# Optimization experiments

Hardware: AMD Instinct MI355X
Metric: run time of the kernel (lower is better)

## Reference

```python
import jax, jax.numpy as jnp
import numpy as np

T = 1024
HID = 2880
H = 64        # query heads
KVH = 8       # kv heads
G = H // KVH  # GQA group size
D = 64        # head dim
WIN = 128     # sliding window
BASE = 150000.0
INIT_CTX = 4096
SCALING = 32.0
NTK_ALPHA = 1.0
NTK_BETA = 32.0
EPS = 1e-5


def _rope_cache():
    # YaRN-style NTK rope cache (scaling_factor > 1 branch), computed in float32.
    d_half = D // 2
    freq = BASE ** (np.arange(0, D, 2, dtype=np.float64) / D)
    concentration = 0.1 * np.log(SCALING) + 1.0
    low = d_half * np.log(INIT_CTX / (NTK_BETA * 2 * np.pi)) / np.log(BASE)
    high = d_half * np.log(INIT_CTX / (NTK_ALPHA * 2 * np.pi)) / np.log(BASE)
    interpolation = 1.0 / (SCALING * freq)
    extrapolation = 1.0 / freq
    ramp = (np.arange(d_half, dtype=np.float64) - low) / (high - low)
    mask = 1.0 - np.clip(ramp, 0.0, 1.0)
    inv_freq = interpolation * (1.0 - mask) + extrapolation * mask
    t = np.arange(INIT_CTX, dtype=np.float64)
    freqs = np.outer(t, inv_freq)                  # [INIT_CTX, D/2]
    cos = (np.cos(freqs) * concentration).astype(np.float32)
    sin = (np.sin(freqs) * concentration).astype(np.float32)
    return jnp.asarray(cos), jnp.asarray(sin)

_COS, _SIN = _rope_cache()


def _apply_rope(x, cos, sin):
    # x: [T, nh, D], cos/sin: [T, D/2]
    c = cos[:, None, :]
    s = sin[:, None, :]
    x1, x2 = jnp.split(x, 2, axis=-1)
    return jnp.concatenate([x1 * c - x2 * s, x2 * c + x1 * s], axis=-1)


def setup_inputs() -> dict:
    key = jax.random.key(0)
    ks = jax.random.split(key, 8)
    hidden_states = jax.random.normal(ks[0], (T, HID), dtype=jnp.float32)
    positions = jnp.arange(T, dtype=jnp.int32)
    norm_scale = jnp.ones((HID,), dtype=jnp.float32)
    qkv_out = H * D + 2 * KVH * D  # 4096 + 512 + 512
    w_qkv = jax.random.normal(ks[1], (HID, qkv_out), dtype=jnp.float32) * (HID ** -0.5)
    b_qkv = jax.random.normal(ks[2], (qkv_out,), dtype=jnp.float32) * 0.01
    w_out = jax.random.normal(ks[3], (H * D, HID), dtype=jnp.float32) * ((H * D) ** -0.5)
    b_out = jax.random.normal(ks[4], (HID,), dtype=jnp.float32) * 0.01
    sinks = jax.random.normal(ks[5], (H,), dtype=jnp.float32)
    return {"hidden_states": hidden_states, "positions": positions,
            "norm_scale": norm_scale, "w_qkv": w_qkv, "b_qkv": b_qkv,
            "w_out": w_out, "b_out": b_out, "sinks": sinks}


def reference(hidden_states, positions, norm_scale, w_qkv, b_qkv, w_out, b_out, sinks):
    # RMSNorm (fp32 math)
    t = hidden_states
    t = t * jax.lax.rsqrt(jnp.mean(t * t, axis=-1, keepdims=True) + EPS)
    t = t * norm_scale

    # fused QKV projection
    qkv = t @ w_qkv + b_qkv
    q = qkv[:, : H * D].reshape(T, H, D)
    k = qkv[:, H * D: H * D + KVH * D].reshape(T, KVH, D)
    v = qkv[:, H * D + KVH * D:].reshape(T, KVH, D)

    # RoPE
    cos = _COS[positions]
    sin = _SIN[positions]
    q = _apply_rope(q, cos, sin)
    k = _apply_rope(k, cos, sin)

    # GQA attention with sliding window + learned sinks
    qg = q.reshape(T, KVH, G, D)
    scale = D ** -0.5
    scores = jnp.einsum('qhgd,khd->hgqk', qg, k) * scale  # [KVH, G, T, T]
    i = jnp.arange(T)[:, None]
    j = jnp.arange(T)[None, :]
    allowed = (j <= i) & (j > i - WIN)  # causal + sliding window
    scores = jnp.where(allowed, scores, -jnp.inf)
    sink = sinks.reshape(KVH, G)[..., None]  # [KVH, G, 1]
    lse = jnp.logaddexp(jax.nn.logsumexp(scores, axis=-1), sink)  # [KVH, G, T]
    probs = jnp.exp(scores - lse[..., None])  # sink mass not attached to any value
    attn = jnp.einsum('hgqk,khd->qhgd', probs, v).reshape(T, H * D)

    out = attn @ w_out + b_out
    return out + hidden_states
```

## Files before the change

### kernel.cpp

```cpp
#include <hip/hip_runtime.h>
#include <hip/hip_bf16.h>
#include <math.h>

#define T_SEQ 1024
#define HIDD 2880
#define NH   64
#define NKVH 8
#define GQ   8
#define HD   64
#define WIN  128
#define QKV_N 5120
#define QDIM  4096
#define KOFF  4096
#define VOFF  4608
#define NPAD_OUT 3072
#define RMS_EPS 1e-5f
#define Z1 3
#define KS1 960
#define Z2 4
#define KS2 1024
#define P1SZ (T_SEQ * QKV_N)
#define P2SZ (T_SEQ * HIDD)

typedef __attribute__((ext_vector_type(8))) short short8;
typedef __attribute__((ext_vector_type(4))) short s16x4;
typedef __attribute__((ext_vector_type(4))) float floatx4;

__device__ __forceinline__ float bf2f(unsigned short u) {
    unsigned int x = ((unsigned int)u) << 16;
    float f; __builtin_memcpy(&f, &x, 4); return f;
}
__device__ __forceinline__ unsigned short f2bf(float f) {
    unsigned int x; __builtin_memcpy(&x, &f, 4);
    unsigned int r = (x + 0x7fffu + ((x >> 16) & 1u)) >> 16;
    return (unsigned short)r;
}
__device__ __forceinline__ void glds16(const unsigned short* g, unsigned short* l) {
    __builtin_amdgcn_global_load_lds(
        (const __attribute__((address_space(1))) void*)g,
        (__attribute__((address_space(3))) void*)l, 16, 0, 0);
}

__global__ __launch_bounds__(256) void prep_kernel(
    const float* __restrict__ w_qkv, const float* __restrict__ w_out,
    const float* __restrict__ hidden, const float* __restrict__ norm_scale,
    const int* __restrict__ positions,
    unsigned short* __restrict__ bqkvT, unsigned short* __restrict__ boutT,
    unsigned short* __restrict__ xn,
    float* __restrict__ tabc, float* __restrict__ tabs)
{
    __shared__ unsigned short tile[64 * 66];
    __shared__ float red[4];
    int blk = blockIdx.x;
    int t = threadIdx.x;

    if (blk < 6672) {
        const float* in; unsigned short* out; int R, C, bx, by;
        if (blk < 3600) { in = w_qkv; out = bqkvT; R = HIDD; C = QKV_N; bx = blk % 80; by = blk / 80; }
        else { int r = blk - 3600; in = w_out; out = boutT; R = QDIM; C = HIDD; bx = r % 48; by = r / 48; }
        int r0 = by * 64, c0 = bx * 64;
        bool inr = (c0 < C);
#pragma unroll
        for (int p = 0; p < 4; ++p) {
            int row = p * 16 + (t >> 4);
            int col = (t & 15) * 4;
            float4 v = inr ? *(const float4*)&in[(size_t)(r0 + row) * C + c0 + col]
                           : make_float4(0.f, 0.f, 0.f, 0.f);
            unsigned int w0 = (unsigned)f2bf(v.x) | ((unsigned)f2bf(v.y) << 16);
            unsigned int w1 = (unsigned)f2bf(v.z) | ((unsigned)f2bf(v.w) << 16);
            *(unsigned int*)&tile[row * 66 + col]     = w0;
            *(unsigned int*)&tile[row * 66 + col + 2] = w1;
        }
        __syncthreads();
        int oc = t >> 2, ks = (t & 3) * 16;
        unsigned short vbuf[16];
#pragma unroll
        for (int j = 0; j < 16; ++j) vbuf[j] = tile[(ks + j) * 66 + oc];
        unsigned short* dst = &out[(size_t)(c0 + oc) * R + r0 + ks];
        *(uint4*)dst       = *(uint4*)&vbuf[0];
        *(uint4*)(dst + 8) = *(uint4*)&vbuf[8];
    } else if (blk < 7696) {
        int row = blk - 6672;
        const float4* hr4 = (const float4*)(hidden + (size_t)row * HIDD);
        const float4* sc4 = (const float4*)norm_scale;
        float ss = 0.f;
        for (int i = t; i < HIDD / 4; i += 256) {
            float4 v = hr4[i];
            ss += v.x * v.x + v.y * v.y + v.z * v.z + v.w * v.w;
        }
        for (int m = 32; m; m >>= 1) ss += __shfl_xor(ss, m, 64);
        if ((t & 63) == 0) red[t >> 6] = ss;
        __syncthreads();
        float tot = red[0] + red[1] + red[2] + red[3];
        float r = rsqrtf(tot / (float)HIDD + RMS_EPS);
        uint2* xr = (uint2*)(xn + (size_t)row * HIDD);
        for (int i = t; i < HIDD / 4; i += 256) {
            float4 v = hr4[i], s4 = sc4[i];
            unsigned int lo = (unsigned)f2bf(v.x * r * s4.x) | ((unsigned)f2bf(v.y * r * s4.y) << 16);
            unsigned int hi = (unsigned)f2bf(v.z * r * s4.z) | ((unsigned)f2bf(v.w * r * s4.w) << 16);
            uint2 o; o.x = lo; o.y = hi;
            xr[i] = o;
        }
    } else {
        int idx = (blk - 7696) * 256 + t;
        int tt = idx >> 5, i = idx & 31;
        double freq = pow(150000.0, (double)(2 * i) / 64.0);
        double lnbase = log(150000.0);
        double low  = 32.0 * log(4096.0 / (32.0 * 2.0 * M_PI)) / lnbase;
        double high = 32.0 * log(4096.0 / (2.0 * M_PI)) / lnbase;
        double ramp = ((double)i - low) / (high - low);
        double mask = 1.0 - fmin(fmax(ramp, 0.0), 1.0);
        double invf = (1.0 / (32.0 * freq)) * (1.0 - mask) + (1.0 / freq) * mask;
        double conc = 0.1 * log(32.0) + 1.0;
        double ang = (double)positions[tt] * invf;
        tabc[idx] = (float)(cos(ang) * conc);
        tabs[idx] = (float)(sin(ang) * conc);
    }
}


#define SYNCPRE() do { \
    __builtin_amdgcn_s_barrier(); \
    asm volatile("s_waitcnt lgkmcnt(0)"); \
    __builtin_amdgcn_s_setprio(1); \
} while (0)
#define SYNCPOST() do { \
    __builtin_amdgcn_s_setprio(0); \
    __builtin_amdgcn_s_barrier(); \
} while (0)

#define LDA_FRAGS(SLOT, QM) do { \
    const unsigned short* _pa = lds + ((SLOT)*4 + (QM)) * 8192 + rowA * 64; \
    _Pragma("unroll") \
    for (int _t = 0; _t < 4; ++_t) { \
        af[_t][0] = *(const short8*)(_pa + _t * 1024 + sl0); \
        af[_t][1] = *(const short8*)(_pa + _t * 1024 + sl1); \
    } \
} while (0)

#define LDB_FRAGS(SLOT, QN, BF) do { \
    const unsigned short* _pb = lds + ((SLOT)*4 + 2 + (QN)) * 8192 + rowB * 64; \
    _Pragma("unroll") \
    for (int _u = 0; _u < 2; ++_u) { \
        BF[_u][0] = *(const short8*)(_pb + _u * 1024 + sl0); \
        BF[_u][1] = *(const short8*)(_pb + _u * 1024 + sl1); \
    } \
} while (0)

#define MFMA_Q(QM, QN, BF) do { \
    _Pragma("unroll") \
    for (int _t = 0; _t < 4; ++_t) { \
        _Pragma("unroll") \
        for (int _u = 0; _u < 2; ++_u) { \
            floatx4 _c = acc[QM][_t][QN][_u]; \
            _c = __builtin_amdgcn_mfma_f32_16x16x32_bf16(af[_t][0], BF[_u][0], _c, 0, 0, 0); \
            _c = __builtin_amdgcn_mfma_f32_16x16x32_bf16(af[_t][1], BF[_u][1], _c, 0, 0, 0); \
            acc[QM][_t][QN][_u] = _c; \
        } \
    } \
} while (0)

#define STAGE(SLOT, MAT, HALF, GP, GR0, KT) do { \
    unsigned short* _d = lds + ((SLOT)*4 + (MAT)*2 + (HALF)) * 8192 + stdst; \
    const unsigned short* _s = (GP) + (size_t)((GR0) + (HALF)*128 + st_r0) * K + kbeg + (KT)*64 + st_c0; \
    glds16(_s, _d); \
    glds16(_s + (size_t)8 * K, _d + 512); \
} while (0)

template <int NX>
__global__ __launch_bounds__(512, 2) void gemm256_kernel(
    const unsigned short* __restrict__ A, const unsigned short* __restrict__ BT,
    unsigned short* __restrict__ P, int M, int N, int K, int Ks)
{
    __shared__ unsigned short lds[65536];

    int b = blockIdx.x;
    int cpx = (int)gridDim.x >> 3;
    int sid = (b & 7) * cpx + (b >> 3);
    int y = sid & 3;
    int xz = sid >> 2;
    int x = xz % NX, z = xz / NX;
    int m0 = y * 256, n0 = x * 256;
    int kbeg = z * Ks;
    int NT = Ks >> 6;
    int NIT = NT >> 1;

    int tid = threadIdx.x;
    int ln = tid & 63, wv = tid >> 6;
    int l16 = ln & 15, quad = ln >> 4;
    int wm = wv >> 2, wn = wv & 3;
    int e8 = l16 & 7;
    int sl0 = ((quad ^ e8) << 3);
    int sl1 = (((4 + quad) ^ e8) << 3);
    int rowA = wm * 64 + l16;
    int rowB = wn * 32 + l16;
    int st_r0 = (wv << 4) + (ln >> 3);
    int st_c0 = (((ln & 7) ^ ((ln >> 3) & 7)) << 3);
    int stdst = (wv << 10) + (ln << 3);

    short8 af[4][2], b0[2][2], b1[2][2];
    floatx4 acc[2][4][2][2];
#pragma unroll
    for (int qm = 0; qm < 2; ++qm)
#pragma unroll
        for (int t = 0; t < 4; ++t)
#pragma unroll
            for (int qn = 0; qn < 2; ++qn)
#pragma unroll
                for (int u = 0; u < 2; ++u)
                    acc[qm][t][qn][u] = (floatx4){0.f, 0.f, 0.f, 0.f};

    STAGE(0, 0, 0, A,  m0, 0); STAGE(0, 0, 1, A,  m0, 0);
    STAGE(0, 1, 0, BT, n0, 0); STAGE(0, 1, 1, BT, n0, 0);
    STAGE(1, 0, 0, A,  m0, 1); STAGE(1, 1, 0, BT, n0, 1);
    asm volatile("s_waitcnt vmcnt(0)");
    __builtin_amdgcn_s_barrier();

    int a = 0;
    for (int i = 0; i < NIT; ++i, a += 2) {
        bool k2 = (a + 2) < NT, k3 = (a + 3) < NT;
        LDA_FRAGS(0, 0); LDB_FRAGS(0, 0, b0);
        STAGE(1, 1, 1, BT, n0, a + 1); STAGE(1, 0, 1, A, m0, a + 1);
        SYNCPRE(); MFMA_Q(0, 0, b0); SYNCPOST();
        LDB_FRAGS(0, 1, b1);
        SYNCPRE(); MFMA_Q(0, 1, b1); SYNCPOST();
        LDA_FRAGS(0, 1);
        if (k2) STAGE(0, 0, 0, A, m0, a + 2);
        SYNCPRE(); MFMA_Q(1, 0, b0); SYNCPOST();
        if (k2) { STAGE(0, 1, 0, BT, n0, a + 2); asm volatile("s_waitcnt vmcnt(8)"); }
        else    { asm volatile("s_waitcnt vmcnt(4)"); }
        SYNCPRE(); MFMA_Q(1, 1, b1); SYNCPOST();
        LDA_FRAGS(1, 0); LDB_FRAGS(1, 0, b0);
        if (k2) { STAGE(0, 1, 1, BT, n0, a + 2); STAGE(0, 0, 1, A, m0, a + 2);
                  asm volatile("s_waitcnt vmcnt(8)"); }
        else    { asm volatile("s_waitcnt vmcnt(0)"); }
        SYNCPRE(); MFMA_Q(0, 0, b0); SYNCPOST();
        LDB_FRAGS(1, 1, b1);
        SYNCPRE(); MFMA_Q(0, 1, b1); SYNCPOST();
        LDA_FRAGS(1, 1);
        if (k3) STAGE(1, 0, 0, A, m0, a + 3);
        SYNCPRE(); MFMA_Q(1, 0, b0); SYNCPOST();
        if (k3) { STAGE(1, 1, 0, BT, n0, a + 3); asm volatile("s_waitcnt vmcnt(4)"); }
        else    { asm volatile("s_waitcnt vmcnt(0)"); }
        SYNCPRE(); MFMA_Q(1, 1, b1); SYNCPOST();
    }
    if (NT & 1) {
        LDA_FRAGS(0, 0); LDB_FRAGS(0, 0, b0);
        SYNCPRE(); MFMA_Q(0, 0, b0); SYNCPOST();
        LDB_FRAGS(0, 1, b1);
        SYNCPRE(); MFMA_Q(0, 1, b1); SYNCPOST();
        LDA_FRAGS(0, 1);
        SYNCPRE(); MFMA_Q(1, 0, b0); SYNCPOST();
        SYNCPRE(); MFMA_Q(1, 1, b1); SYNCPOST();
    }

    unsigned short* Pz = P + (size_t)z * M * N;
#pragma unroll
    for (int qm = 0; qm < 2; ++qm)
#pragma unroll
        for (int t = 0; t < 4; ++t) {
            int rbase = m0 + qm * 128 + wm * 64 + t * 16 + quad * 4;
#pragma unroll
            for (int qn = 0; qn < 2; ++qn)
#pragma unroll
                for (int u = 0; u < 2; ++u) {
                    int col = n0 + qn * 128 + wn * 32 + u * 16 + l16;
                    if (col < N) {
#pragma unroll
                        for (int r = 0; r < 4; ++r)
                            Pz[(size_t)(rbase + r) * N + col] = f2bf(acc[qm][t][qn][u][r]);
                    }
                }
        }
}

__global__ __launch_bounds__(256) void reduce_out_kernel(
    const unsigned short* __restrict__ P, const float* __restrict__ bias,
    const float* __restrict__ resid, float* __restrict__ out)
{
    int idx = (blockIdx.x * 256 + threadIdx.x) * 4;
    int n = idx % HIDD;
    float4 rv = *(const float4*)(resid + idx);
    float4 bv = *(const float4*)(bias + n);
    float a0 = bv.x + rv.x, a1 = bv.y + rv.y, a2 = bv.z + rv.z, a3 = bv.w + rv.w;
#pragma unroll
    for (int z = 0; z < Z2; ++z) {
        s16x4 p = *(const s16x4*)(P + (size_t)z * P2SZ + idx);
        a0 += bf2f((unsigned short)p[0]);
        a1 += bf2f((unsigned short)p[1]);
        a2 += bf2f((unsigned short)p[2]);
        a3 += bf2f((unsigned short)p[3]);
    }
    float4 ov = {a0, a1, a2, a3};
    *(float4*)(out + idx) = ov;
}

__global__ __launch_bounds__(512) void attn_kernel(
    const unsigned short* __restrict__ P1, const float* __restrict__ b_qkv,
    const float* __restrict__ sinks,
    const float* __restrict__ tabc, const float* __restrict__ tabs,
    unsigned short* __restrict__ attn)
{
    int i0 = blockIdx.x * 16;
    int kh = blockIdx.y;
    int tid = threadIdx.x, lane = tid & 63, g = tid >> 6;
    int quad = lane >> 4, l16 = lane & 15;
    int tile_j0 = i0 - 127;

    __shared__ unsigned short sU[8 * 16 * 168];
    __shared__ unsigned short sVt[64 * 168];
    unsigned short* sK = sU;
    unsigned short* sPw = sU + g * 16 * 168;

    {
        int d = lane, dd = lane & 31;
        float kb1 = b_qkv[KOFF + kh * 64 + d];
        float kb2 = b_qkv[KOFF + kh * 64 + (d ^ 32)];
        float vb  = b_qkv[VOFF + kh * 64 + d];
        for (int it = 0; it < 18; ++it) {
            int s = it * 8 + g;
            int j = tile_j0 + s;
            unsigned short kst = 0, vst = 0;
            if (j >= 0 && j < T_SEQ) {
                size_t ko = (size_t)j * QKV_N + KOFF + kh * 64;
                float x1 = kb1, x2 = kb2, vv = vb;
#pragma unroll
                for (int z = 0; z < Z1; ++z) {
                    const unsigned short* Pz = P1 + (size_t)z * P1SZ;
                    x1 += bf2f(Pz[ko + d]);
                    x2 += bf2f(Pz[ko + (d ^ 32)]);
                    vv += bf2f(Pz[ko + 512 + d]);
                }
                float c = tabc[j * 32 + dd], sn = tabs[j * 32 + dd];
                kst = f2bf((d < 32) ? (x1 * c - x2 * sn) : (x1 * c + x2 * sn));
                vst = f2bf(vv);
            }
            sK[s * 72 + d] = kst;
            sVt[d * 168 + s] = vst;
        }
        sVt[d * 168 + 144 + 2 * g]     = 0;
        sVt[d * 168 + 144 + 2 * g + 1] = 0;
    }

    int qi = i0 + l16;
    int hb = (kh * GQ + g) * 64;
    short8 qa, qb;
    {
        size_t qo = (size_t)qi * QKV_N + hb + quad * 8;
        float x1[8], x2[8];
#pragma unroll
        for (int j = 0; j < 8; ++j) {
            x1[j] = b_qkv[hb + quad * 8 + j];
            x2[j] = b_qkv[hb + quad * 8 + 32 + j];
        }
#pragma unroll
        for (int z = 0; z < Z1; ++z) {
            const unsigned short* Pz = P1 + (size_t)z * P1SZ;
            short8 lo = *(const short8*)(Pz + qo);
            short8 hi = *(const short8*)(Pz + qo + 32);
#pragma unroll
            for (int j = 0; j < 8; ++j) {
                x1[j] += bf2f((unsigned short)lo[j]);
                x2[j] += bf2f((unsigned short)hi[j]);
            }
        }
        const float* cc = tabc + qi * 32 + quad * 8;
        const float* sc = tabs + qi * 32 + quad * 8;
#pragma unroll
        for (int j = 0; j < 8; ++j) {
            float c = cc[j] * 0.125f, sn = sc[j] * 0.125f;
            qa[j] = (short)f2bf(x1[j] * c - x2[j] * sn);
            qb[j] = (short)f2bf(x2[j] * c + x1[j] * sn);
        }
    }
    __syncthreads();

    floatx4 Sc[9];
#pragma unroll
    for (int nt = 0; nt < 9; ++nt) Sc[nt] = (floatx4){0.f, 0.f, 0.f, 0.f};
#pragma unroll
    for (int nt = 0; nt < 9; ++nt) {
        short8 kb0 = *(const short8*)&sK[(nt * 16 + l16) * 72 + quad * 8];
        short8 kb1 = *(const short8*)&sK[(nt * 16 + l16) * 72 + 32 + quad * 8];
        Sc[nt] = __builtin_amdgcn_mfma_f32_16x16x32_bf16(qa, kb0, Sc[nt], 0, 0, 0);
        Sc[nt] = __builtin_amdgcn_mfma_f32_16x16x32_bf16(qb, kb1, Sc[nt], 0, 0, 0);
    }

    int smin = 127 - i0;
    float mx[4], sm[4], inv[4];
#pragma unroll
    for (int r = 0; r < 4; ++r) {
        int qoff = quad * 4 + r;
        int lo = qoff > smin ? qoff : smin;
        int hi = qoff + 127;
        float m = -INFINITY;
#pragma unroll
        for (int nt = 0; nt < 9; ++nt) {
            int s = nt * 16 + l16;
            float v = (s >= lo && s <= hi) ? Sc[nt][r] : -INFINITY;
            Sc[nt][r] = v;
            m = fmaxf(m, v);
        }
        mx[r] = m;
    }
#pragma unroll
    for (int mmask = 1; mmask < 16; mmask <<= 1)
#pragma unroll
        for (int r = 0; r < 4; ++r)
            mx[r] = fmaxf(mx[r], __shfl_xor(mx[r], mmask, 64));
    float sink = sinks[kh * GQ + g];
#pragma unroll
    for (int r = 0; r < 4; ++r) {
        mx[r] = fmaxf(mx[r], sink);
        float s = 0.f;
#pragma unroll
        for (int nt = 0; nt < 9; ++nt) {
            float p = __expf(Sc[nt][r] - mx[r]);
            Sc[nt][r] = p;
            s += p;
        }
        sm[r] = s;
    }
#pragma unroll
    for (int mmask = 1; mmask < 16; mmask <<= 1)
#pragma unroll
        for (int r = 0; r < 4; ++r)
            sm[r] += __shfl_xor(sm[r], mmask, 64);
#pragma unroll
    for (int r = 0; r < 4; ++r)
        inv[r] = 1.f / (sm[r] + __expf(sink - mx[r]));

    __syncthreads();

#pragma unroll
    for (int nt = 0; nt < 9; ++nt)
#pragma unroll
        for (int r = 0; r < 4; ++r)
            sPw[(quad * 4 + r) * 168 + nt * 16 + l16] = f2bf(Sc[nt][r]);
    {
        int q = lane >> 2, so = (lane & 3) * 4;
        *(s16x4*)&sPw[q * 168 + 144 + so] = (s16x4){0, 0, 0, 0};
    }

    floatx4 O[4];
#pragma unroll
    for (int nt = 0; nt < 4; ++nt) O[nt] = (floatx4){0.f, 0.f, 0.f, 0.f};
#pragma unroll
    for (int kt = 0; kt < 5; ++kt) {
        short8 pa = *(const short8*)&sPw[l16 * 168 + kt * 32 + quad * 8];
#pragma unroll
        for (int nt = 0; nt < 4; ++nt) {
            short8 vb = *(const short8*)&sVt[(nt * 16 + l16) * 168 + kt * 32 + quad * 8];
            O[nt] = __builtin_amdgcn_mfma_f32_16x16x32_bf16(pa, vb, O[nt], 0, 0, 0);
        }
    }
#pragma unroll
    for (int nt = 0; nt < 4; ++nt)
#pragma unroll
        for (int r = 0; r < 4; ++r) {
            int q = quad * 4 + r;
            attn[(size_t)(i0 + q) * QDIM + (kh * GQ + g) * 64 + nt * 16 + l16] =
                f2bf(O[nt][r] * inv[r]);
        }
}

extern "C" void kernel_launch(void* const* d_in, const int* in_sizes, int n_in,
                              void* d_out, int out_size, void* d_ws, size_t ws_size,
                              hipStream_t stream)
{
    const float* hidden     = (const float*)d_in[0];
    const int*   positions  = (const int*)d_in[1];
    const float* norm_scale = (const float*)d_in[2];
    const float* w_qkv      = (const float*)d_in[3];
    const float* b_qkv      = (const float*)d_in[4];
    const float* w_out      = (const float*)d_in[5];
    const float* b_out      = (const float*)d_in[6];
    const float* sinks      = (const float*)d_in[7];
    float* out = (float*)d_out;

    char* ws = (char*)d_ws;
    float*          tabc  = (float*)ws;
    float*          tabs  = (float*)(ws + 131072);
    unsigned short* boutT = (unsigned short*)(ws + 262144);
    unsigned short* xn    = (unsigned short*)(ws + 25427968);
    unsigned short* bqkvT = (unsigned short*)(ws + 31326208);
    unsigned short* P1    = (unsigned short*)(ws + 60817408);
    unsigned short* attnb = (unsigned short*)(ws + 25427968);
    unsigned short* P2    = (unsigned short*)(ws + 60817408);

    prep_kernel<<<7824, 256, 0, stream>>>(
        w_qkv, w_out, hidden, norm_scale, positions, bqkvT, boutT, xn, tabc, tabs);
    gemm256_kernel<20><<<4 * 20 * Z1, 512, 0, stream>>>(
        xn, bqkvT, P1, T_SEQ, QKV_N, HIDD, KS1);
    attn_kernel<<<dim3(T_SEQ / 16, NKVH), 512, 0, stream>>>(
        P1, b_qkv, sinks, tabc, tabs, attnb);
    gemm256_kernel<12><<<4 * 12 * Z2, 512, 0, stream>>>(
        attnb, boutT, P2, T_SEQ, HIDD, QDIM, KS2);
    reduce_out_kernel<<<2880, 256, 0, stream>>>(P2, b_out, hidden, out);
}
```

Measured before the change: 254.9 us.

## Vectorize K/V staging in attention, re-split out-proj K, use float rope trig

The K/V tile staging in the attention kernel now has each thread load 8 or 16 contiguous bf16 values with 128-bit loads and write K rows with vector LDS stores. Before, each thread handled one scalar element per row, and K and V were interleaved across threads. The output-projection split-K changes from 4 slices of 1024 to 5 slices of 832, and the GEMM clamps the last slice to the remaining K. The rope table now reduces the angle in double and evaluates cosf/sinf in float instead of double cos/sin, which lowers trig cost but can shift table values slightly.

```diff
diff --git a/kernel.cpp b/kernel.cpp
--- a/kernel.cpp
+++ b/kernel.cpp
@@ -17,8 +17,8 @@
 #define RMS_EPS 1e-5f
 #define Z1 3
 #define KS1 960
-#define Z2 4
-#define KS2 1024
+#define Z2 5
+#define KS2 832
 #define P1SZ (T_SEQ * QKV_N)
 #define P2SZ (T_SEQ * HIDD)
 
@@ -113,8 +113,10 @@
         double invf = (1.0 / (32.0 * freq)) * (1.0 - mask) + (1.0 / freq) * mask;
         double conc = 0.1 * log(32.0) + 1.0;
         double ang = (double)positions[tt] * invf;
-        tabc[idx] = (float)(cos(ang) * conc);
-        tabs[idx] = (float)(sin(ang) * conc);
+        double tw = floor(ang * (1.0 / (2.0 * M_PI)));
+        float ar = (float)(ang - tw * (2.0 * M_PI));
+        tabc[idx] = cosf(ar) * (float)conc;
+        tabs[idx] = sinf(ar) * (float)conc;
     }
 }
 
@@ -182,7 +184,8 @@
     int x = xz % NX, z = xz / NX;
     int m0 = y * 256, n0 = x * 256;
     int kbeg = z * Ks;
-    int NT = Ks >> 6;
+    int kslice = K - kbeg; if (kslice > Ks) kslice = Ks;
+    int NT = kslice >> 6;
     int NIT = NT >> 1;
 
     int tid = threadIdx.x;
@@ -313,33 +316,91 @@
     unsigned short* sPw = sU + g * 16 * 168;
 
     {
-        int d = lane, dd = lane & 31;
-        float kb1 = b_qkv[KOFF + kh * 64 + d];
-        float kb2 = b_qkv[KOFF + kh * 64 + (d ^ 32)];
-        float vb  = b_qkv[VOFF + kh * 64 + d];
-        for (int it = 0; it < 18; ++it) {
-            int s = it * 8 + g;
-            int j = tile_j0 + s;
-            unsigned short kst = 0, vst = 0;
-            if (j >= 0 && j < T_SEQ) {
-                size_t ko = (size_t)j * QKV_N + KOFF + kh * 64;
-                float x1 = kb1, x2 = kb2, vv = vb;
-#pragma unroll
-                for (int z = 0; z < Z1; ++z) {
-                    const unsigned short* Pz = P1 + (size_t)z * P1SZ;
-                    x1 += bf2f(Pz[ko + d]);
-                    x2 += bf2f(Pz[ko + (d ^ 32)]);
-                    vv += bf2f(Pz[ko + 512 + d]);
+        int rs = tid >> 3;
+        int c  = tid & 7;
+        if (c < 4) {
+            int d0 = c * 8;
+            float kb1[8], kb2[8];
+#pragma unroll
+            for (int jj = 0; jj < 8; ++jj) {
+                kb1[jj] = b_qkv[KOFF + kh * 64 + d0 + jj];
+                kb2[jj] = b_qkv[KOFF + kh * 64 + d0 + 32 + jj];
+            }
+            for (int it = 0; it < 3; ++it) {
+                int s = it * 64 + rs;
+                if (s < 144) {
+                    int j = tile_j0 + s;
+                    unsigned short olo[8], ohi[8];
+                    if (j >= 0 && j < T_SEQ) {
+                        float x1[8], x2[8];
+#pragma unroll
+                        for (int jj = 0; jj < 8; ++jj) { x1[jj] = kb1[jj]; x2[jj] = kb2[jj]; }
+                        size_t ko = (size_t)j * QKV_N + KOFF + kh * 64 + d0;
+#pragma unroll
+                        for (int z = 0; z < Z1; ++z) {
+                            const unsigned short* Pz = P1 + (size_t)z * P1SZ;
+                            short8 lo = *(const short8*)(Pz + ko);
+                            short8 hi = *(const short8*)(Pz + ko + 32);
+#pragma unroll
+                            for (int jj = 0; jj < 8; ++jj) {
+                                x1[jj] += bf2f((unsigned short)lo[jj]);
+                                x2[jj] += bf2f((unsigned short)hi[jj]);
+                            }
+                        }
+                        const float* cc = tabc + j * 32 + d0;
+                        const float* sc = tabs + j * 32 + d0;
+#pragma unroll
+                        for (int jj = 0; jj < 8; ++jj) {
+                            float cj = cc[jj], sj = sc[jj];
+                            olo[jj] = f2bf(x1[jj] * cj - x2[jj] * sj);
+                            ohi[jj] = f2bf(x2[jj] * cj + x1[jj] * sj);
+                        }
+                    } else {
+#pragma unroll
+                        for (int jj = 0; jj < 8; ++jj) { olo[jj] = 0; ohi[jj] = 0; }
+                    }
+                    *(uint4*)&sK[s * 72 + d0]      = *(uint4*)olo;
+                    *(uint4*)&sK[s * 72 + 32 + d0] = *(uint4*)ohi;
                 }
-                float c = tabc[j * 32 + dd], sn = tabs[j * 32 + dd];
-                kst = f2bf((d < 32) ? (x1 * c - x2 * sn) : (x1 * c + x2 * sn));
-                vst = f2bf(vv);
             }
-            sK[s * 72 + d] = kst;
-            sVt[d * 168 + s] = vst;
-        }
-        sVt[d * 168 + 144 + 2 * g]     = 0;
-        sVt[d * 168 + 144 + 2 * g + 1] = 0;
+        } else {
+            int d0 = (c - 4) * 16;
+            float vbi[16];
+#pragma unroll
+            for (int jj = 0; jj < 16; ++jj) vbi[jj] = b_qkv[VOFF + kh * 64 + d0 + jj];
+            for (int it = 0; it < 3; ++it) {
+                int s = it * 64 + rs;
+                if (s < 144) {
+                    int j = tile_j0 + s;
+                    if (j >= 0 && j < T_SEQ) {
+                        float vv[16];
+#pragma unroll
+                        for (int jj = 0; jj < 16; ++jj) vv[jj] = vbi[jj];
+                        size_t ko = (size_t)j * QKV_N + VOFF + kh * 64 + d0;
+#pragma unroll
+                        for (int z = 0; z < Z1; ++z) {
+                            const unsigned short* Pz = P1 + (size_t)z * P1SZ;
+                            short8 lo = *(const short8*)(Pz + ko);
+                            short8 hi = *(const short8*)(Pz + ko + 8);
+#pragma unroll
+                            for (int jj = 0; jj < 8; ++jj) {
+                                vv[jj]     += bf2f((unsigned short)lo[jj]);
+                                vv[8 + jj] += bf2f((unsigned short)hi[jj]);
+                            }
+                        }
+#pragma unroll
+                        for (int jj = 0; jj < 16; ++jj)
+                            sVt[(d0 + jj) * 168 + s] = f2bf(vv[jj]);
+                    } else {
+#pragma unroll
+                        for (int jj = 0; jj < 16; ++jj)
+                            sVt[(d0 + jj) * 168 + s] = 0;
+                    }
+                }
+            }
+        }
+        int zd = tid >> 3, zc = 144 + (tid & 7) * 2;
+        *(unsigned int*)&sVt[zd * 168 + zc] = 0;
     }
 
     int qi = i0 + l16;
```

Result: faster. 249.4 us (-2.2%).
